# Kernel tuning notes

Hardware: AMD Instinct MI355X
Metric: run time of the kernel (lower is better)

The kernel has to match this reference:

```python
import jax, jax.numpy as jnp
import numpy as np

N = 100000   # nodes
E = 1600000  # edges
F_IN = 128   # node_features
H = 64       # hidden_features


def setup_inputs() -> dict:
    key = jax.random.key(0)
    ks = jax.random.split(key, 16)
    s = 0.05
    return {
        "x": jax.random.normal(ks[0], (N, F_IN), dtype=jnp.float32),
        "edge_index": jax.random.randint(ks[1], (2, E), 0, N, dtype=jnp.int64),
        "W1": jax.random.normal(ks[2], (H, F_IN), dtype=jnp.float32) * s,
        "b1": jnp.zeros((H,), dtype=jnp.float32),
        "W2": jax.random.normal(ks[3], (H, H), dtype=jnp.float32) * s,
        "b2": jnp.zeros((H,), dtype=jnp.float32),
        "Wk": jax.random.normal(ks[4], (H, H), dtype=jnp.float32) * s,
        "bk": jnp.zeros((H,), dtype=jnp.float32),
        "Wq": jax.random.normal(ks[5], (H, H), dtype=jnp.float32) * s,
        "bq": jnp.zeros((H,), dtype=jnp.float32),
        "Wv": jax.random.normal(ks[6], (H, H), dtype=jnp.float32) * s,
        "bv": jnp.zeros((H,), dtype=jnp.float32),
        "Ws": jax.random.normal(ks[7], (H, H), dtype=jnp.float32) * s,  # lin_skip, bias=False
        "b_gate": jnp.zeros((H,), dtype=jnp.float32),                   # conv bias param
        "Wsc": jax.random.normal(ks[8], (1, H), dtype=jnp.float32) * s,
        "bsc": jnp.zeros((1,), dtype=jnp.float32),
    }


def reference(x, edge_index, W1, b1, W2, b2, Wk, bk, Wq, bq, Wv, bv, Ws, b_gate, Wsc, bsc):
    # MLP front-end: Linear + ReLU + Linear
    h = jax.nn.relu(x @ W1.T + b1)
    h = h @ W2.T + b2                      # [N, H]

    # ResGatedGraphConv (sum aggregation, sigmoid gating)
    k = h @ Wk.T + bk                      # key on destination nodes
    q = h @ Wq.T + bq                      # query on source nodes
    v = h @ Wv.T + bv                      # value on source nodes

    src = edge_index[0]                    # j
    dst = edge_index[1]                    # i
    # message_ij = sigmoid(k_i + q_j) * v_j, scatter-add to destination i
    msg = jax.nn.sigmoid(k[dst] + q[src]) * v[src]   # [E, H]
    agg = jax.ops.segment_sum(msg, dst, num_segments=N)

    out = agg + h @ Ws.T + b_gate          # root skip (no bias) + conv bias

    # scorer head
    score = out @ Wsc.T + bsc              # [N, 1]
    return score
```

## Files before the change

### kernel.cpp

```cpp
#include <hip/hip_runtime.h>

#define HD  64
#define FIN 128

#define WS_W1H   0
#define WS_W1L   4096
#define WS_MALL  8192
#define WS_BK    14848
#define WS_BQ    14912
#define WS_BVW   14976
#define WS_BASE  15040
#define WS_K     15104

#define BSHIFT 7
#define BSIZE  128
#define CHUNK  3200
#define MAXNPB 512
#define CAP2   3072

#define C1f  3.9026344e-3f
#define C3f  (-7.67612e-8f)
#define C5f  1.2236660e-12f

typedef __attribute__((ext_vector_type(8))) short short8;
typedef __attribute__((ext_vector_type(4))) float f32x4;

__device__ __forceinline__ unsigned bf16rne(float f) {
    unsigned u = __float_as_uint(f);
    unsigned r = ((u >> 16) & 1u) + 0x7fffu;
    return (u + r) >> 16;
}
__device__ __forceinline__ float blo(unsigned u) { return __uint_as_float(u << 16); }
__device__ __forceinline__ float bhi(unsigned u) { return __uint_as_float(u & 0xffff0000u); }

__device__ __forceinline__ float grp4(unsigned ku, unsigned qu, unsigned va,
                                      unsigned vb, float p) {
    #pragma unroll
    for (int i = 0; i < 4; ++i) {
        float kf = (float)((ku >> (8 * i)) & 255u);
        float qf = (float)((qu >> (8 * i)) & 255u);
        unsigned vu = (i < 2) ? va : vb;
        float vf = (i & 1) ? bhi(vu) : blo(vu);
        float xx = kf + qf;
        xx = fminf(fmaxf(xx, 128.f), 384.f);
        float sv = xx - 256.f;
        float z = sv * sv;
        float w = fmaf(z, C5f, C3f);
        w = fmaf(z, w, C1f);
        p = fmaf(vf * sv, w, p);
        p = fmaf(vf, 0.5f, p);
    }
    return p;
}

__global__ void gnn_prep(const float* __restrict__ W1, const float* __restrict__ W2,
                         const float* __restrict__ b2,
                         const float* __restrict__ Wk, const float* __restrict__ bk,
                         const float* __restrict__ Wq, const float* __restrict__ bq,
                         const float* __restrict__ Wv, const float* __restrict__ bv,
                         const float* __restrict__ Wsm, const float* __restrict__ Wsc,
                         const float* __restrict__ bgate, const float* __restrict__ bsc,
                         float* __restrict__ ws) {
    __shared__ float w2s[4096];
    __shared__ float wxsT[65 * 64];
    int b = blockIdx.x, t = threadIdx.x;
    unsigned short* w1h  = (unsigned short*)(ws + WS_W1H);
    unsigned short* w1l  = (unsigned short*)(ws + WS_W1L);
    unsigned short* mall = (unsigned short*)(ws + WS_MALL);
    if (b == 0) {
        for (int idx = t; idx < HD * FIN; idx += blockDim.x) {
            float v = W1[idx];
            unsigned u = __float_as_uint(v);
            w1h[idx] = (unsigned short)(u >> 16);
            float rem = v - __uint_as_float(u & 0xffff0000u);
            w1l[idx] = (unsigned short)bf16rne(rem);
        }
    } else if (b <= 12) {
        int m = (b - 1) >> 2, qtr = (b - 1) & 3;
        const float* Wx = (m == 0) ? Wk : (m == 1) ? Wq : Wv;
        const float* bx = (m == 0) ? bk : (m == 1) ? bq : bv;
        int boffw = (m == 0) ? WS_BK : (m == 1) ? WS_BQ : WS_BVW;
        for (int i = t * 4; i < 4096; i += 1024)
            *(float4*)&w2s[i] = *(const float4*)&W2[i];
        for (int idx = t; idx < 4096; idx += 256) {
            int o = idx >> 6, c = idx & 63;
            wxsT[c * 65 + o] = Wx[idx];
        }
        __syncthreads();
        for (int idx = t; idx < 1024; idx += 256) {
            int a = qtr * 16 + (idx >> 6), o = idx & 63;
            float acc = 0.f;
            for (int c = 0; c < HD; ++c) acc += w2s[c * HD + a] * wxsT[c * 65 + o];
            if (m == 2) acc *= Wsc[o];
            mall[(m * 64 + o) * HD + a] = (unsigned short)bf16rne(acc);
        }
        if (qtr == 0 && t < HD) {
            float acc = bx[t];
            for (int c = 0; c < HD; ++c) acc += b2[c] * wxsT[c * 65 + t];
            if (m == 2) acc *= Wsc[t];
            ws[boffw + t] = acc;
        }
    } else {
        __shared__ float wsk[HD];
        if (t < HD) {
            float a = 0.f;
            for (int d = 0; d < HD; ++d) a += Wsm[d * HD + t] * Wsc[d];
            wsk[t] = a;
        }
        __syncthreads();
        if (t < HD) {
            float a = 0.f;
            for (int c = 0; c < HD; ++c) a += W2[c * HD + t] * wsk[c];
            mall[192 * HD + t] = (unsigned short)bf16rne(a);
        }
        for (int idx = t; idx < 15 * HD; idx += 256)
            mall[193 * HD + idx] = 0;
        if (t == 0) {
            float a = bsc[0];
            for (int d = 0; d < HD; ++d) a += bgate[d] * Wsc[d];
            float acc2 = 0.f;
            for (int c = 0; c < HD; ++c) {
                float wk2 = 0.f;
                for (int d = 0; d < HD; ++d) wk2 += Wsm[d * HD + c] * Wsc[d];
                acc2 += b2[c] * wk2;
            }
            ws[WS_BASE] = a + acc2;
        }
    }
}

__global__ __launch_bounds__(256, 2) void gnn_part(const int* __restrict__ ei,
                                                   unsigned* __restrict__ ebuf,
                                                   int* __restrict__ dir,
                                                   int E, int NPB, int nbkt) {
    __shared__ unsigned spk[CHUNK];
    __shared__ unsigned srt[CHUNK];
    __shared__ unsigned short sbk[CHUNK];
    __shared__ int off[1024], curx[1024], prt[256];
    int t = threadIdx.x, blk = blockIdx.x;
    int base = blk * CHUNK;
    int n = min(CHUNK, E - base);

    #pragma unroll
    for (int i = 0; i < 4; ++i) off[t * 4 + i] = 0;
    __syncthreads();

    for (int i = t; i < n; i += 256) {
        int src = ei[base + i], dst = ei[E + base + i];
        spk[i] = (unsigned)src | ((unsigned)(dst & (BSIZE - 1)) << 17);
        int b = dst >> BSHIFT;
        sbk[i] = (unsigned short)b;
        atomicAdd(&off[b], 1);
    }
    __syncthreads();

    int h0 = off[4 * t], h1 = off[4 * t + 1], h2 = off[4 * t + 2], h3 = off[4 * t + 3];
    int tot = h0 + h1 + h2 + h3;
    prt[t] = tot;
    __syncthreads();
    for (int s = 1; s < 256; s <<= 1) {
        int v = (t >= s) ? prt[t - s] : 0;
        __syncthreads();
        prt[t] += v;
        __syncthreads();
    }
    int excl = prt[t] - tot;
    off[4 * t] = excl;                    curx[4 * t] = excl;
    off[4 * t + 1] = excl + h0;           curx[4 * t + 1] = excl + h0;
    off[4 * t + 2] = excl + h0 + h1;      curx[4 * t + 2] = excl + h0 + h1;
    off[4 * t + 3] = excl + h0 + h1 + h2; curx[4 * t + 3] = excl + h0 + h1 + h2;
    __syncthreads();

    for (int i = t; i < n; i += 256) {
        int r = atomicAdd(&curx[sbk[i]], 1);
        srt[r] = spk[i];
    }
    __syncthreads();

    for (int i = t; i < n; i += 256)
        ebuf[base + i] = srt[i];
    for (int bb = t; bb <= nbkt; bb += 256)
        dir[bb * NPB + blk] = base + off[bb];
}

__global__ __launch_bounds__(256, 3) void gnn_node(const float* __restrict__ x,
                                                   const float* __restrict__ b1,
                                                   const float* __restrict__ ws,
                                                   uint4* __restrict__ karr,
                                                   uint4* __restrict__ qv,
                                                   float* __restrict__ score, int N) {
    __shared__ __align__(16) char smem[32768];
    char* XHb = smem;
    char* XLb = smem + 16384;

    int tid = threadIdx.x;
    int l = tid & 63, w = tid >> 6;
    int nbase = blockIdx.x * 64;

    #pragma unroll
    for (int it = 0; it < 8; ++it) {
        int idx = it * 64 + l;
        int nl = 16 * w + (idx >> 5);
        int c4 = idx & 31;
        int node = min(nbase + nl, N - 1);
        float4 v = ((const float4*)x)[(size_t)node * 32 + c4];
        unsigned u0 = __float_as_uint(v.x), u1 = __float_as_uint(v.y);
        unsigned u2 = __float_as_uint(v.z), u3 = __float_as_uint(v.w);
        uint2 hx, lx;
        hx.x = (u0 >> 16) | (u1 & 0xffff0000u);
        hx.y = (u2 >> 16) | (u3 & 0xffff0000u);
        float r0 = v.x - __uint_as_float(u0 & 0xffff0000u);
        float r1 = v.y - __uint_as_float(u1 & 0xffff0000u);
        float r2 = v.z - __uint_as_float(u2 & 0xffff0000u);
        float r3 = v.w - __uint_as_float(u3 & 0xffff0000u);
        lx.x = bf16rne(r0) | (bf16rne(r1) << 16);
        lx.y = bf16rne(r2) | (bf16rne(r3) << 16);
        int bo = (nl * 256 + c4 * 8) ^ ((nl & 7) << 4);
        *(uint2*)(XHb + bo) = hx;
        *(uint2*)(XLb + bo) = lx;
    }
    __syncthreads();

    int rl = l & 15, kb = l >> 4;
    int rowA = 16 * w + rl;
    int swzA = (rowA & 7) << 4;

    const unsigned short* w1h = (const unsigned short*)(ws + WS_W1H);
    const unsigned short* w1l = (const unsigned short*)(ws + WS_W1L);
    f32x4 acc1[4];
    #pragma unroll
    for (int t = 0; t < 4; ++t) {
        float bv = b1[t * 16 + rl];
        acc1[t] = (f32x4){bv, bv, bv, bv};
    }
    #pragma unroll
    for (int s = 0; s < 4; ++s) {
        int abyte = (rowA * 256 + s * 64 + kb * 16) ^ swzA;
        short8 ah = *(const short8*)(XHb + abyte);
        short8 al = *(const short8*)(XLb + abyte);
        int koff = s * 32 + kb * 8;
        #pragma unroll
        for (int t = 0; t < 4; ++t) {
            int col = t * 16 + rl;
            short8 bh = *(const short8*)&w1h[col * FIN + koff];
            short8 bl = *(const short8*)&w1l[col * FIN + koff];
            acc1[t] = __builtin_amdgcn_mfma_f32_16x16x32_bf16(ah, bh, acc1[t], 0, 0, 0);
            acc1[t] = __builtin_amdgcn_mfma_f32_16x16x32_bf16(al, bh, acc1[t], 0, 0, 0);
            acc1[t] = __builtin_amdgcn_mfma_f32_16x16x32_bf16(ah, bl, acc1[t], 0, 0, 0);
        }
    }
    __syncthreads();

    int r0w = (l >> 4) * 4;
    #pragma unroll
    for (int t = 0; t < 4; ++t) {
        int col = t * 16 + rl;
        #pragma unroll
        for (int r = 0; r < 4; ++r) {
            int row = 16 * w + r0w + r;
            float v = fmaxf(acc1[t][r], 0.f);
            int hb = (row * 128 + col * 2) ^ ((row & 7) << 4);
            *(unsigned short*)(smem + hb) = (unsigned short)bf16rne(v);
        }
    }
    __syncthreads();

    const unsigned short* mall = (const unsigned short*)(ws + WS_MALL);
    const float* bK = ws + WS_BK;
    const float* bQ = ws + WS_BQ;
    const float* bV = ws + WS_BVW;
    float base = ws[WS_BASE];
    f32x4 acc2[13];
    #pragma unroll
    for (int t = 0; t < 4; ++t) {
        float v = bK[t * 16 + rl];
        acc2[t] = (f32x4){v, v, v, v};
    }
    #pragma unroll
    for (int t = 0; t < 4; ++t) {
        float v = bQ[t * 16 + rl];
        acc2[4 + t] = (f32x4){v, v, v, v};
    }
    #pragma unroll
    for (int t = 0; t < 4; ++t) {
        float v = bV[t * 16 + rl];
        acc2[8 + t] = (f32x4){v, v, v, v};
    }
    acc2[12] = (f32x4){0.f, 0.f, 0.f, 0.f};

    #pragma unroll
    for (int s = 0; s < 2; ++s) {
        int abyte = (rowA * 128 + (s * 32 + kb * 8) * 2) ^ swzA;
        short8 a = *(const short8*)(smem + abyte);
        int koff = s * 32 + kb * 8;
        #pragma unroll
        for (int t = 0; t < 13; ++t) {
            short8 b = *(const short8*)&mall[(t * 16 + rl) * HD + koff];
            acc2[t] = __builtin_amdgcn_mfma_f32_16x16x32_bf16(a, b, acc2[t], 0, 0, 0);
        }
    }

    char* Ku = smem + 16384;
    char* Qu = smem + 20480;
    char* VW = smem + 24576;
    #pragma unroll
    for (int t = 0; t < 4; ++t) {
        int col = t * 16 + rl;
        #pragma unroll
        for (int r = 0; r < 4; ++r) {
            int row = 16 * w + r0w + r;
            int ek = min(max(__float2int_rn(fmaf(acc2[t][r],     64.f, 128.f)), 0), 255);
            int eq = min(max(__float2int_rn(fmaf(acc2[4 + t][r], 64.f, 128.f)), 0), 255);
            Ku[row * 64 + col] = (char)ek;
            Qu[row * 64 + col] = (char)eq;
            *(unsigned short*)(VW + row * 128 + col * 2) =
                (unsigned short)bf16rne(acc2[8 + t][r]);
        }
    }
    if (rl == 0) {
        #pragma unroll
        for (int r = 0; r < 4; ++r) {
            int node = nbase + 16 * w + r0w + r;
            if (node < N) score[node] = base + acc2[12][r];
        }
    }
    __syncthreads();

    {
        int n = tid >> 2, p = tid & 3;
        int node = nbase + n;
        if (node < N)
            karr[(size_t)node * 4 + p] = *(const uint4*)(Ku + n * 64 + p * 16);
    }
    #pragma unroll
    for (int it = 0; it < 3; ++it) {
        int n = tid >> 2, p = (tid & 3) + it * 4;
        int node = nbase + n;
        const char* srcp = (p < 4) ? (Qu + n * 64 + p * 16)
                                   : (VW + n * 128 + (p - 4) * 16);
        if (node < N) qv[(size_t)node * 12 + p] = *(const uint4*)srcp;
    }
}

__global__ __launch_bounds__(256, 4) void gnn_bsort(const unsigned* __restrict__ ebuf,
                                                    const int* __restrict__ dir,
                                                    unsigned* __restrict__ ebuf2,
                                                    int* __restrict__ dir2,
                                                    int NPB, int WINDIV) {
    __shared__ unsigned ebl[CAP2];
    __shared__ int rs[MAXNPB], tl[MAXNPB], pf[MAXNPB + 1], part[256];
    __shared__ int hw[8], woff[9], wcur[8];
    int tid = threadIdx.x, db = blockIdx.x;

    for (int i = tid; i < NPB; i += 256) {
        int s = dir[db * NPB + i];
        rs[i] = s;
        tl[i] = dir[(db + 1) * NPB + i] - s;
    }
    if (tid < 8) hw[tid] = 0;
    __syncthreads();

    int i0 = 2 * tid, i1 = 2 * tid + 1;
    int l0 = (i0 < NPB) ? tl[i0] : 0;
    int l1 = (i1 < NPB) ? tl[i1] : 0;
    part[tid] = l0 + l1;
    __syncthreads();
    for (int s = 1; s < 256; s <<= 1) {
        int v = (tid >= s) ? part[tid - s] : 0;
        __syncthreads();
        part[tid] += v;
        __syncthreads();
    }
    int excl = part[tid] - (l0 + l1);
    if (i0 <= NPB) pf[i0] = excl;
    if (i1 <= NPB) pf[i1] = excl + l0;
    if (tid == 255) pf[NPB] = part[255];
    __syncthreads();
    int cnt = min(pf[NPB], CAP2);

    for (int r = tid; r < NPB; r += 256) {
        int s = rs[r], o = pf[r], n = tl[r];
        for (int j = 0; j < n; ++j) {
            int d = o + j;
            if (d < CAP2) ebl[d] = ebuf[s + j];
        }
    }
    __syncthreads();

    for (int i = tid; i < cnt; i += 256) {
        int w = (int)((ebl[i] & 0x1FFFFu) / (unsigned)WINDIV);
        atomicAdd(&hw[min(w, 7)], 1);
    }
    __syncthreads();
    if (tid == 0) {
        int s = 0;
        #pragma unroll
        for (int w = 0; w < 8; ++w) { woff[w] = s; wcur[w] = s; s += hw[w]; }
        woff[8] = s;
    }
    __syncthreads();

    for (int i = tid; i < cnt; i += 256) {
        unsigned pk = ebl[i];
        int w = min((int)((pk & 0x1FFFFu) / (unsigned)WINDIV), 7);
        int r = atomicAdd(&wcur[w], 1);
        ebuf2[(size_t)db * CAP2 + r] = pk;
    }
    if (tid <= 8) dir2[db * 9 + tid] = woff[tid];
}

__global__ __launch_bounds__(256, 8) void gnn_edge(const unsigned* __restrict__ ebuf2,
                                                   const int* __restrict__ dir2,
                                                   const uint4* __restrict__ karr,
                                                   const uint4* __restrict__ qv,
                                                   float* __restrict__ partial, int N) {
    __shared__ float accumF[BSIZE];
    int tid = threadIdx.x;
    int win = blockIdx.x & 7, db = blockIdx.x >> 3;
    int s = dir2[db * 9 + win], e2 = dir2[db * 9 + win + 1];
    size_t base = (size_t)db * CAP2;

    if (tid < BSIZE) accumF[tid] = 0.f;
    __syncthreads();

    int q = tid >> 2, f = tid & 3;
    for (int i = s + q; i < e2; i += 64) {
        unsigned pk = ebuf2[base + i];
        int src = (int)(pk & 0x1FFFFu);
        int dl = (int)(pk >> 17) & (BSIZE - 1);
        int dst = (db << BSHIFT) + dl;
        uint4 ku = karr[(size_t)dst * 4 + f];
        uint4 qu = qv[(size_t)src * 12 + f];
        uint4 va = qv[(size_t)src * 12 + 4 + 2 * f];
        uint4 vb = qv[(size_t)src * 12 + 5 + 2 * f];
        float p = 0.f;
        p = grp4(ku.x, qu.x, va.x, va.y, p);
        p = grp4(ku.y, qu.y, va.z, va.w, p);
        p = grp4(ku.z, qu.z, vb.x, vb.y, p);
        p = grp4(ku.w, qu.w, vb.z, vb.w, p);
        p += __shfl_down(p, 2, 4);
        p += __shfl_down(p, 1, 4);
        if (f == 0) atomicAdd(&accumF[dl], p);
    }
    __syncthreads();
    if (tid < BSIZE) {
        int node = (db << BSHIFT) + tid;
        if (node < N) partial[(size_t)win * N + node] = accumF[tid];
    }
}

__global__ __launch_bounds__(256) void gnn_final(const float* __restrict__ partial,
                                                 float* __restrict__ score, int N) {
    int n = blockIdx.x * 256 + threadIdx.x;
    if (n < N) {
        float s = score[n];
        #pragma unroll
        for (int w = 0; w < 8; ++w) s += partial[(size_t)w * N + n];
        score[n] = s;
    }
}

extern "C" void kernel_launch(void* const* d_in, const int* in_sizes, int n_in,
                              void* d_out, int out_size, void* d_ws, size_t ws_size,
                              hipStream_t stream) {
    const float* x    = (const float*)d_in[0];
    const int*   ei   = (const int*)d_in[1];
    const float* W1   = (const float*)d_in[2];
    const float* b1   = (const float*)d_in[3];
    const float* W2   = (const float*)d_in[4];
    const float* b2   = (const float*)d_in[5];
    const float* Wk   = (const float*)d_in[6];
    const float* bk   = (const float*)d_in[7];
    const float* Wq   = (const float*)d_in[8];
    const float* bq   = (const float*)d_in[9];
    const float* Wv   = (const float*)d_in[10];
    const float* bv   = (const float*)d_in[11];
    const float* Wsm  = (const float*)d_in[12];
    const float* bgat = (const float*)d_in[13];
    const float* Wsc  = (const float*)d_in[14];
    const float* bsc  = (const float*)d_in[15];

    int N = in_sizes[0] / FIN;
    int E = in_sizes[1] / 2;

    float* ws      = (float*)d_ws;
    float* karr    = ws + WS_K;
    float* qvarr   = karr + (size_t)N * 16;
    unsigned* ebuf = (unsigned*)(qvarr + (size_t)N * 48);
    int nbkt = (N + BSIZE - 1) >> BSHIFT;
    int NPB  = (E + CHUNK - 1) / CHUNK;
    int* dir = (int*)(ebuf + (size_t)E);
    unsigned* ebuf2 = (unsigned*)(dir + (size_t)(nbkt + 1) * NPB);
    int* dir2 = (int*)(ebuf2 + (size_t)nbkt * CAP2);
    float* partial = (float*)ebuf;
    float* score = (float*)d_out;

    int NB = (N + 63) / 64;
    int WINDIV = (N + 7) / 8;

    gnn_prep<<<14, 256, 0, stream>>>(W1, W2, b2, Wk, bk, Wq, bq, Wv, bv,
                                     Wsm, Wsc, bgat, bsc, ws);
    gnn_part<<<NPB, 256, 0, stream>>>(ei, ebuf, dir, E, NPB, nbkt);
    gnn_bsort<<<nbkt, 256, 0, stream>>>(ebuf, dir, ebuf2, dir2, NPB, WINDIV);
    gnn_node<<<NB, 256, 0, stream>>>(x, b1, ws, (uint4*)karr, (uint4*)qvarr,
                                     score, N);
    gnn_edge<<<nbkt * 8, 256, 0, stream>>>(ebuf2, dir2, (const uint4*)karr,
                                           (const uint4*)qvarr, partial, N);
    gnn_final<<<(N + 255) / 256, 256, 0, stream>>>(partial, score, N);
}
```

Measured before the change: 278.6 us.

## Partition node-projection MFMA work by output columns across waves to reuse weight fragments

Each wave now owns a slice of output columns for all 64 rows instead of 16 rows across all columns. It loads each weight B-fragment once and reuses it across four row tiles, while the A-fragments come from shared memory. The 13 output tiles of the second GEMM are spread round-robin across the four waves. This cuts per-wave global/L2 weight fragment loads, but adds more shared-memory A reads and leaves the second-GEMM work unbalanced across waves.

```diff
diff --git a/kernel.cpp b/kernel.cpp
--- a/kernel.cpp
+++ b/kernel.cpp
@@ -222,81 +222,79 @@
     __syncthreads();
 
     int rl = l & 15, kb = l >> 4;
-    int rowA = 16 * w + rl;
-    int swzA = (rowA & 7) << 4;
+    int swz = (rl & 7) << 4;
+    int r0w = kb * 4;
 
     const unsigned short* w1h = (const unsigned short*)(ws + WS_W1H);
     const unsigned short* w1l = (const unsigned short*)(ws + WS_W1L);
+    int colW = 16 * w + rl;
+    float bv1 = b1[colW];
     f32x4 acc1[4];
     #pragma unroll
-    for (int t = 0; t < 4; ++t) {
-        float bv = b1[t * 16 + rl];
-        acc1[t] = (f32x4){bv, bv, bv, bv};
-    }
+    for (int m = 0; m < 4; ++m) acc1[m] = (f32x4){bv1, bv1, bv1, bv1};
+
     #pragma unroll
     for (int s = 0; s < 4; ++s) {
-        int abyte = (rowA * 256 + s * 64 + kb * 16) ^ swzA;
-        short8 ah = *(const short8*)(XHb + abyte);
-        short8 al = *(const short8*)(XLb + abyte);
         int koff = s * 32 + kb * 8;
-        #pragma unroll
-        for (int t = 0; t < 4; ++t) {
-            int col = t * 16 + rl;
-            short8 bh = *(const short8*)&w1h[col * FIN + koff];
-            short8 bl = *(const short8*)&w1l[col * FIN + koff];
-            acc1[t] = __builtin_amdgcn_mfma_f32_16x16x32_bf16(ah, bh, acc1[t], 0, 0, 0);
-            acc1[t] = __builtin_amdgcn_mfma_f32_16x16x32_bf16(al, bh, acc1[t], 0, 0, 0);
-            acc1[t] = __builtin_amdgcn_mfma_f32_16x16x32_bf16(ah, bl, acc1[t], 0, 0, 0);
-        }
-    }
-    __syncthreads();
-
-    int r0w = (l >> 4) * 4;
-    #pragma unroll
-    for (int t = 0; t < 4; ++t) {
-        int col = t * 16 + rl;
+        short8 bh = *(const short8*)&w1h[colW * FIN + koff];
+        short8 bl = *(const short8*)&w1l[colW * FIN + koff];
+        #pragma unroll
+        for (int m = 0; m < 4; ++m) {
+            int abyte = ((m * 16 + rl) * 256 + s * 64 + kb * 16) ^ swz;
+            short8 ah = *(const short8*)(XHb + abyte);
+            short8 al = *(const short8*)(XLb + abyte);
+            acc1[m] = __builtin_amdgcn_mfma_f32_16x16x32_bf16(ah, bh, acc1[m], 0, 0, 0);
+            acc1[m] = __builtin_amdgcn_mfma_f32_16x16x32_bf16(al, bh, acc1[m], 0, 0, 0);
+            acc1[m] = __builtin_amdgcn_mfma_f32_16x16x32_bf16(ah, bl, acc1[m], 0, 0, 0);
+        }
+    }
+    __syncthreads();
+
+    #pragma unroll
+    for (int m = 0; m < 4; ++m) {
         #pragma unroll
         for (int r = 0; r < 4; ++r) {
-            int row = 16 * w + r0w + r;
-            float v = fmaxf(acc1[t][r], 0.f);
-            int hb = (row * 128 + col * 2) ^ ((row & 7) << 4);
+            int row = m * 16 + r0w + r;
+            float v = fmaxf(acc1[m][r], 0.f);
+            int hb = (row * 128 + colW * 2) ^ ((row & 7) << 4);
             *(unsigned short*)(smem + hb) = (unsigned short)bf16rne(v);
         }
     }
     __syncthreads();
 
     const unsigned short* mall = (const unsigned short*)(ws + WS_MALL);
-    const float* bK = ws + WS_BK;
-    const float* bQ = ws + WS_BQ;
-    const float* bV = ws + WS_BVW;
     float base = ws[WS_BASE];
-    f32x4 acc2[13];
-    #pragma unroll
-    for (int t = 0; t < 4; ++t) {
-        float v = bK[t * 16 + rl];
-        acc2[t] = (f32x4){v, v, v, v};
-    }
-    #pragma unroll
-    for (int t = 0; t < 4; ++t) {
-        float v = bQ[t * 16 + rl];
-        acc2[4 + t] = (f32x4){v, v, v, v};
-    }
-    #pragma unroll
-    for (int t = 0; t < 4; ++t) {
-        float v = bV[t * 16 + rl];
-        acc2[8 + t] = (f32x4){v, v, v, v};
-    }
-    acc2[12] = (f32x4){0.f, 0.f, 0.f, 0.f};
+    f32x4 acc2[4][4];
+    #pragma unroll
+    for (int j = 0; j < 4; ++j) {
+        int t = 4 * j + w;
+        float iv = 0.f;
+        if (t < 4)       iv = ws[WS_BK  + t * 16 + rl];
+        else if (t < 8)  iv = ws[WS_BQ  + (t - 4) * 16 + rl];
+        else if (t < 12) iv = ws[WS_BVW + (t - 8) * 16 + rl];
+        #pragma unroll
+        for (int m = 0; m < 4; ++m) acc2[m][j] = (f32x4){iv, iv, iv, iv};
+    }
 
     #pragma unroll
     for (int s = 0; s < 2; ++s) {
-        int abyte = (rowA * 128 + (s * 32 + kb * 8) * 2) ^ swzA;
-        short8 a = *(const short8*)(smem + abyte);
         int koff = s * 32 + kb * 8;
-        #pragma unroll
-        for (int t = 0; t < 13; ++t) {
-            short8 b = *(const short8*)&mall[(t * 16 + rl) * HD + koff];
-            acc2[t] = __builtin_amdgcn_mfma_f32_16x16x32_bf16(a, b, acc2[t], 0, 0, 0);
+        short8 a[4];
+        #pragma unroll
+        for (int m = 0; m < 4; ++m) {
+            int abyte = ((m * 16 + rl) * 128 + koff * 2) ^ swz;
+            a[m] = *(const short8*)(smem + abyte);
+        }
+        #pragma unroll
+        for (int j = 0; j < 4; ++j) {
+            int t = 4 * j + w;
+            if (t <= 12) {
+                short8 b = *(const short8*)&mall[(t * 16 + rl) * HD + koff];
+                #pragma unroll
+                for (int m = 0; m < 4; ++m)
+                    acc2[m][j] = __builtin_amdgcn_mfma_f32_16x16x32_bf16(a[m], b,
+                                                                acc2[m][j], 0, 0, 0);
+            }
         }
     }
 
@@ -304,24 +302,29 @@
     char* Qu = smem + 20480;
     char* VW = smem + 24576;
     #pragma unroll
-    for (int t = 0; t < 4; ++t) {
-        int col = t * 16 + rl;
-        #pragma unroll
-        for (int r = 0; r < 4; ++r) {
-            int row = 16 * w + r0w + r;
-            int ek = min(max(__float2int_rn(fmaf(acc2[t][r],     64.f, 128.f)), 0), 255);
-            int eq = min(max(__float2int_rn(fmaf(acc2[4 + t][r], 64.f, 128.f)), 0), 255);
-            Ku[row * 64 + col] = (char)ek;
-            Qu[row * 64 + col] = (char)eq;
-            *(unsigned short*)(VW + row * 128 + col * 2) =
-                (unsigned short)bf16rne(acc2[8 + t][r]);
-        }
-    }
-    if (rl == 0) {
-        #pragma unroll
-        for (int r = 0; r < 4; ++r) {
-            int node = nbase + 16 * w + r0w + r;
-            if (node < N) score[node] = base + acc2[12][r];
+    for (int j = 0; j < 4; ++j) {
+        int t = 4 * j + w;
+        if (t > 12) continue;
+        #pragma unroll
+        for (int m = 0; m < 4; ++m) {
+            #pragma unroll
+            for (int r = 0; r < 4; ++r) {
+                int row = m * 16 + r0w + r;
+                float v = acc2[m][j][r];
+                if (t < 4) {
+                    int e = min(max(__float2int_rn(fmaf(v, 64.f, 128.f)), 0), 255);
+                    Ku[row * 64 + t * 16 + rl] = (char)e;
+                } else if (t < 8) {
+                    int e = min(max(__float2int_rn(fmaf(v, 64.f, 128.f)), 0), 255);
+                    Qu[row * 64 + (t - 4) * 16 + rl] = (char)e;
+                } else if (t < 12) {
+                    *(unsigned short*)(VW + row * 128 + ((t - 8) * 16 + rl) * 2) =
+                        (unsigned short)bf16rne(v);
+                } else if (rl == 0) {
+                    int node = nbase + row;
+                    if (node < N) score[node] = base + v;
+                }
+            }
         }
     }
     __syncthreads();
```

Result: faster. 249.1 us (-10.6%).
